# Performance work log

Hardware: AMD Instinct MI355X
Metric: run time of the kernel (lower is better)

## Reference

```python
import jax, jax.numpy as jnp
import numpy as np

N = 100000      # nodes
E = 1600000     # edges (avg degree 16)
D_IN, D_H, D_OUT = 128, 128, 64


def setup_inputs() -> dict:
    key = jax.random.key(0)
    k1, k2, k3, k4 = jax.random.split(key, 4)
    x = jax.random.normal(k1, (N, D_IN), dtype=jnp.float32)
    edge_index = jax.random.randint(k2, (2, E), 0, N, dtype=jnp.int32)
    W1 = jax.random.normal(k3, (D_IN, D_H), dtype=jnp.float32) * (1.0 / np.sqrt(D_IN))
    b1 = jnp.zeros((D_H,), dtype=jnp.float32)
    W2 = jax.random.normal(k4, (D_H, D_OUT), dtype=jnp.float32) * (1.0 / np.sqrt(D_H))
    b2 = jnp.zeros((D_OUT,), dtype=jnp.float32)
    return {"x": x, "edge_index": edge_index, "W1": W1, "b1": b1, "W2": W2, "b2": b2}


def _gcn_conv(x, src, dst, W, b):
    """PyG GCNConv: out = D^{-1/2} (A + I) D^{-1/2} (x W) + b."""
    n = x.shape[0]
    h = x @ W  # [N, D_out] — transform first, then aggregate (PyG order)
    loops = jnp.arange(n, dtype=src.dtype)
    src_f = jnp.concatenate([src, loops])
    dst_f = jnp.concatenate([dst, loops])
    deg = jax.ops.segment_sum(jnp.ones_like(dst_f, dtype=h.dtype), dst_f, num_segments=n)
    dinv = jax.lax.rsqrt(deg)  # deg >= 1 due to self-loops
    norm = dinv[src_f] * dinv[dst_f]            # [E+N]
    msg = h[src_f] * norm[:, None]              # [E+N, D_out] gather
    out = jax.ops.segment_sum(msg, dst_f, num_segments=n)  # scatter-add
    return out + b


def reference(x, edge_index, W1, b1, W2, b2):
    src, dst = edge_index[0], edge_index[1]
    h = jax.nn.relu(_gcn_conv(x, src, dst, W1, b1))
    o = _gcn_conv(h, src, dst, W2, b2)
    return jax.nn.log_softmax(o, axis=1)
```

## Files before the change

kernel.cpp:

```cpp
#include <hip/hip_runtime.h>
#include <hip/hip_bf16.h>

typedef __hip_bfloat16 bf16;
typedef short short8 __attribute__((ext_vector_type(8)));
typedef float f32x4 __attribute__((ext_vector_type(4)));
typedef float f32x2 __attribute__((ext_vector_type(2)));

#define NPB 256
#define MAXBUK 1024

__device__ __forceinline__ float bf2f_raw(unsigned short u) {
    unsigned x = ((unsigned)u) << 16; float f; __builtin_memcpy(&f, &x, 4); return f;
}
__device__ __forceinline__ unsigned short f2bf_raw(float f) {
    unsigned u; __builtin_memcpy(&u, &f, 4);
    u += 0x7FFFu + ((u >> 16) & 1u);
    return (unsigned short)(u >> 16);
}
__device__ __forceinline__ float lo_f(unsigned u) {
    unsigned x = u << 16; float f; __builtin_memcpy(&f, &x, 4); return f;
}
__device__ __forceinline__ float hi_f(unsigned u) {
    unsigned x = u & 0xffff0000u; float f; __builtin_memcpy(&f, &x, 4); return f;
}


__global__ __launch_bounds__(256) void fatA_kernel(const unsigned short* __restrict__ W1s,
                                                   const void* __restrict__ W1p,
                                                   const void* __restrict__ W2p,
                                                   const void* __restrict__ b1p,
                                                   const void* __restrict__ b2p,
                                                   unsigned short* __restrict__ WB1,
                                                   unsigned short* __restrict__ WB2,
                                                   float* __restrict__ b1f,
                                                   float* __restrict__ b2f,
                                                   int* __restrict__ flag, int nshorts,
                                                   const int* __restrict__ dst,
                                                   int* __restrict__ bktcnt,
                                                   int E, int nbuk, int prepb) {
    __shared__ int smem[MAXBUK];
    const int tt = threadIdx.x;
    if ((int)blockIdx.x < prepb) {
        const int sample = min(nshorts, 2048);
        int c = 0;
        for (int i = tt; i < sample; i += 256) {
            unsigned e = (W1s[i] >> 7) & 0xFFu;
            if (e >= 140u || (e >= 1u && e <= 40u)) c++;
        }
        smem[tt] = c;
        __syncthreads();
        for (int o = 128; o > 0; o >>= 1) {
            if (tt < o) smem[tt] += smem[tt + o];
            __syncthreads();
        }
        const int isf32 = (smem[0] > sample / 8) ? 1 : 0;
        if (blockIdx.x == 0 && tt == 0) *flag = isf32;

        const int t = blockIdx.x * 256 + tt;
        const int T1 = 16384, T2 = 8192;
        if (t < T1) {
            int j = t & 7, l = (t >> 3) & 63, f = t >> 9;
            int n = f >> 2, kk = f & 3;
            int k = kk * 32 + (l >> 4) * 8 + j;
            int col = n * 16 + (l & 15);
            WB1[t] = isf32 ? f2bf_raw(((const float*)W1p)[k * 128 + col])
                           : ((const unsigned short*)W1p)[k * 128 + col];
        } else if (t < T1 + T2) {
            int o = t - T1;
            int j = o & 7, l = (o >> 3) & 63, f = o >> 9;
            int n = f >> 2, kk = f & 3;
            int k = kk * 32 + (l >> 4) * 8 + j;
            int col = n * 16 + (l & 15);
            WB2[o] = isf32 ? f2bf_raw(((const float*)W2p)[k * 64 + col])
                           : ((const unsigned short*)W2p)[k * 64 + col];
        } else if (t < T1 + T2 + 128) {
            int o = t - T1 - T2;
            b1f[o] = isf32 ? ((const float*)b1p)[o] : bf2f_raw(((const unsigned short*)b1p)[o]);
        } else if (t < T1 + T2 + 192) {
            int o = t - T1 - T2 - 128;
            b2f[o] = isf32 ? ((const float*)b2p)[o] : bf2f_raw(((const unsigned short*)b2p)[o]);
        }
    } else {
        const int e0 = ((int)blockIdx.x - prepb) * 4096;
        const int e1 = min(E, e0 + 4096);
        for (int b = tt; b < nbuk; b += 256) smem[b] = 0;
        __syncthreads();
        for (int e = e0 + tt; e < e1; e += 256) atomicAdd(&smem[dst[e] >> 8], 1);
        __syncthreads();
        for (int b = tt; b < nbuk; b += 256) {
            int c = smem[b];
            if (c) atomicAdd(&bktcnt[b], c);
        }
    }
}

__global__ __launch_bounds__(1024) void bscan_kernel(const int* __restrict__ bktcnt,
                                                     int* __restrict__ bofs,
                                                     int* __restrict__ bcur,
                                                     int nbuk, int total) {
    __shared__ int ps[1024];
    const int t = threadIdx.x;
    int v = (t < nbuk) ? bktcnt[t] : 0;
    ps[t] = v;
    __syncthreads();
    for (int o = 1; o < 1024; o <<= 1) {
        int u = (t >= o) ? ps[t - o] : 0;
        __syncthreads();
        ps[t] += u;
        __syncthreads();
    }
    if (t < nbuk) {
        int ex = ps[t] - v;
        bofs[t] = ex;
        bcur[t] = ex;
    }
    if (t == 0) bofs[nbuk] = total;
}


__global__ __launch_bounds__(256) void fatB_kernel(const void* __restrict__ Xp,
                                                   const unsigned short* __restrict__ WB1,
                                                   unsigned char* __restrict__ Hf8, int nrows,
                                                   const int* __restrict__ flag,
                                                   const int* __restrict__ src,
                                                   const int* __restrict__ dst,
                                                   int* __restrict__ bcur,
                                                   unsigned* __restrict__ packed,
                                                   int E, int nbuk, int gb) {
    __shared__ __align__(16) char smem[34816];
    const int t = threadIdx.x;
    if ((int)blockIdx.x < gb) {
        unsigned short* Xs = (unsigned short*)smem;
        unsigned short* Cs = (unsigned short*)smem;
        const int r0 = blockIdx.x * 128;
        const int isf32 = *flag;

        if (isf32) {
            const float4* Xg = (const float4*)Xp;
            #pragma unroll
            for (int i = 0; i < 16; ++i) {
                int idx = t + 256 * i;
                int row = idx >> 5, c4 = idx & 31;
                float4 v = {0.f, 0.f, 0.f, 0.f};
                if (r0 + row < nrows) v = Xg[(size_t)(r0 + row) * 32 + c4];
                unsigned lo = (unsigned)f2bf_raw(v.x) | ((unsigned)f2bf_raw(v.y) << 16);
                unsigned hi = (unsigned)f2bf_raw(v.z) | ((unsigned)f2bf_raw(v.w) << 16);
                *reinterpret_cast<uint2*>(&Xs[row * 136 + c4 * 4]) = make_uint2(lo, hi);
            }
        } else {
            const uint4* Xg = (const uint4*)Xp;
            #pragma unroll
            for (int i = 0; i < 8; ++i) {
                int idx = t + 256 * i;
                int row = idx >> 4, c8 = idx & 15;
                uint4 v = {0u, 0u, 0u, 0u};
                if (r0 + row < nrows) v = Xg[(size_t)(r0 + row) * 16 + c8];
                *reinterpret_cast<uint4*>(&Xs[row * 136 + c8 * 8]) = v;
            }
        }
        __syncthreads();

        const int lane = t & 63, w = t >> 6;
        const int m0 = w * 32;
        short8 a[2][4];
        #pragma unroll
        for (int rt = 0; rt < 2; ++rt)
            #pragma unroll
            for (int kk = 0; kk < 4; ++kk)
                a[rt][kk] = *reinterpret_cast<const short8*>(
                    &Xs[(m0 + rt * 16 + (lane & 15)) * 136 + kk * 32 + (lane >> 4) * 8]);
        __syncthreads();

        for (int p = 0; p < 2; ++p) {
            short8 b[4][4];
            #pragma unroll
            for (int n = 0; n < 4; ++n)
                #pragma unroll
                for (int kk = 0; kk < 4; ++kk)
                    b[n][kk] = *reinterpret_cast<const short8*>(
                        WB1 + (size_t)(((p * 4 + n) * 4 + kk) * 64 + lane) * 8);
            f32x4 acc[2][4];
            #pragma unroll
            for (int rt = 0; rt < 2; ++rt)
                #pragma unroll
                for (int n = 0; n < 4; ++n) {
                    acc[rt][n] = (f32x4){0.f, 0.f, 0.f, 0.f};
                    #pragma unroll
                    for (int kk = 0; kk < 4; ++kk)
                        acc[rt][n] = __builtin_amdgcn_mfma_f32_16x16x32_bf16(
                            a[rt][kk], b[n][kk], acc[rt][n], 0, 0, 0);
                }
            if (p) __syncthreads();
            #pragma unroll
            for (int rt = 0; rt < 2; ++rt)
                #pragma unroll
                for (int n = 0; n < 4; ++n)
                    #pragma unroll
                    for (int r = 0; r < 4; ++r) {
                        int row = m0 + rt * 16 + (lane >> 4) * 4 + r;
                        Cs[row * 68 + n * 16 + (lane & 15)] = f2bf_raw(acc[rt][n][r]);
                    }
            __syncthreads();
            #pragma unroll
            for (int i = 0; i < 4; ++i) {
                int idx = t + 256 * i;
                int row = idx >> 3, c8 = idx & 7;
                if (r0 + row < nrows) {
                    uint2 va = *reinterpret_cast<const uint2*>(&Cs[row * 68 + c8 * 8]);
                    uint2 vb = *reinterpret_cast<const uint2*>(&Cs[row * 68 + c8 * 8 + 4]);
                    int w0 = __builtin_amdgcn_cvt_pk_fp8_f32(lo_f(va.x), hi_f(va.x), 0, false);
                    w0 = __builtin_amdgcn_cvt_pk_fp8_f32(lo_f(va.y), hi_f(va.y), w0, true);
                    int w1 = __builtin_amdgcn_cvt_pk_fp8_f32(lo_f(vb.x), hi_f(vb.x), 0, false);
                    w1 = __builtin_amdgcn_cvt_pk_fp8_f32(lo_f(vb.y), hi_f(vb.y), w1, true);
                    *reinterpret_cast<uint2*>(Hf8 + (size_t)(r0 + row) * 128 + p * 64 + c8 * 8) =
                        make_uint2((unsigned)w0, (unsigned)w1);
                }
            }
            if (!p) __syncthreads();
        }
    } else {
        int* cnt = (int*)smem;
        int* gbase = (int*)(smem + 4096);
        const int e0 = ((int)blockIdx.x - gb) * 4096;
        const int e1 = min(E, e0 + 4096);
        for (int b = t; b < nbuk; b += 256) cnt[b] = 0;
        __syncthreads();
        for (int e = e0 + t; e < e1; e += 256) atomicAdd(&cnt[dst[e] >> 8], 1);
        __syncthreads();
        for (int b = t; b < nbuk; b += 256) {
            int c = cnt[b];
            gbase[b] = c ? atomicAdd(&bcur[b], c) : 0;
            cnt[b] = 0;
        }
        __syncthreads();
        for (int e = e0 + t; e < e1; e += 256) {
            int d = dst[e];
            int b = d >> 8;
            int r = atomicAdd(&cnt[b], 1);
            packed[gbase[b] + r] = ((unsigned)(d & 255) << 24) | (unsigned)src[e];
        }
    }
}

__global__ __launch_bounds__(256) void csr_fine2_kernel(const unsigned* __restrict__ packed,
                                                        const int* __restrict__ bofs,
                                                        uint2* __restrict__ nmeta,
                                                        float* __restrict__ dinv,
                                                        unsigned* __restrict__ epu, int n) {
    __shared__ int cnt2[NPB];
    __shared__ int cur[NPB];
    const int t = threadIdx.x;
    const int b = blockIdx.x;
    const int node0 = b << 8;
    const int nn = min(NPB, n - node0);
    cnt2[t] = 0;
    __syncthreads();
    const int beg = bofs[b], end = bofs[b + 1];
    for (int i = beg + t; i < end; i += 256) atomicAdd(&cnt2[packed[i] >> 24], 1);
    __syncthreads();
    int c = cnt2[t];
    cur[t] = c;
    __syncthreads();
    for (int o = 1; o < 256; o <<= 1) {
        int u = (t >= o) ? cur[t - o] : 0;
        __syncthreads();
        cur[t] += u;
        __syncthreads();
    }
    const int base = beg + cur[t] - c;
    if (t < nn) {
        nmeta[node0 + t] = make_uint2((unsigned)base, (unsigned)c);
        dinv[node0 + t] = rsqrtf((float)(c + 1));
    }
    __syncthreads();
    cur[t] = base;
    __syncthreads();
    for (int i = beg + t; i < end; i += 256) {
        unsigned u = packed[i];
        int pos = atomicAdd(&cur[u >> 24], 1);
        epu[2 * pos] = u & 0xFFFFFFu;
    }
}

__global__ __launch_bounds__(256) void epw_kernel(unsigned* __restrict__ epu,
                                                  const float* __restrict__ dinv, int E) {
    int i = blockIdx.x * 256 + threadIdx.x;
    if (i < E) {
        unsigned s = epu[2 * i];
        float w = dinv[s];
        unsigned wb; __builtin_memcpy(&wb, &w, 4);
        epu[2 * i + 1] = wb;
    }
}


__device__ __forceinline__ float epw_f(uint2 e) {
    float w; __builtin_memcpy(&w, &e.y, 4); return w;
}

__device__ __forceinline__ void accf8_2(f32x2* acc, uint2 v, float w) {
    f32x2 wv = {w, w};
    acc[0] += __builtin_amdgcn_cvt_pk_f32_fp8(v.x, false) * wv;
    acc[1] += __builtin_amdgcn_cvt_pk_f32_fp8(v.x, true)  * wv;
    acc[2] += __builtin_amdgcn_cvt_pk_f32_fp8(v.y, false) * wv;
    acc[3] += __builtin_amdgcn_cvt_pk_f32_fp8(v.y, true)  * wv;
}

__global__ __launch_bounds__(128) void agg128_v9(const uint2* __restrict__ H2,
                                                 const uint2* __restrict__ nmeta,
                                                 const uint2* __restrict__ epack,
                                                 const float* __restrict__ biasf,
                                                 uint4* __restrict__ G4, int n) {
    const int lane = threadIdx.x & 63;
    const int g = lane >> 4;
    const int sub = lane & 15;
    const int node = blockIdx.x * 2 + (threadIdx.x >> 6);
    if (node >= n) return;

    uint2 vself = H2[((unsigned)node << 4) + (unsigned)sub];

    const uint2 meta = nmeta[node];
    const int base = (int)meta.x;
    const int cnt = (int)meta.y;
    const int end = base + cnt;
    const float di = rsqrtf((float)(cnt + 1));

    f32x2 acc[4];
    #pragma unroll
    for (int i = 0; i < 4; ++i) acc[i] = (f32x2){0.f, 0.f};
    accf8_2(acc, vself, (g == 0) ? di : 0.f);

    int j = base;
    for (; j + 15 < end; j += 16) {
        uint2 e0 = epack[j + g];
        uint2 e1 = epack[j + 4 + g];
        uint2 e2 = epack[j + 8 + g];
        uint2 e3 = epack[j + 12 + g];
        uint2 v0 = H2[(e0.x << 4) + (unsigned)sub];
        uint2 v1 = H2[(e1.x << 4) + (unsigned)sub];
        uint2 v2 = H2[(e2.x << 4) + (unsigned)sub];
        uint2 v3 = H2[(e3.x << 4) + (unsigned)sub];
        accf8_2(acc, v0, epw_f(e0));
        accf8_2(acc, v1, epw_f(e1));
        accf8_2(acc, v2, epw_f(e2));
        accf8_2(acc, v3, epw_f(e3));
    }
    for (; j + 7 < end; j += 8) {
        uint2 e0 = epack[j + g];
        uint2 e1 = epack[j + 4 + g];
        uint2 v0 = H2[(e0.x << 4) + (unsigned)sub];
        uint2 v1 = H2[(e1.x << 4) + (unsigned)sub];
        accf8_2(acc, v0, epw_f(e0));
        accf8_2(acc, v1, epw_f(e1));
    }
    for (; j + 3 < end; j += 4) {
        uint2 e0 = epack[j + g];
        uint2 v0 = H2[(e0.x << 4) + (unsigned)sub];
        accf8_2(acc, v0, epw_f(e0));
    }
    if (j + g < end) {
        uint2 e0 = epack[j + g];
        uint2 v0 = H2[(e0.x << 4) + (unsigned)sub];
        accf8_2(acc, v0, epw_f(e0));
    }

    float a8[8];
    #pragma unroll
    for (int i = 0; i < 4; ++i) { a8[2 * i] = acc[i].x; a8[2 * i + 1] = acc[i].y; }
    #pragma unroll
    for (int i = 0; i < 8; ++i) {
        a8[i] += __shfl_xor(a8[i], 16, 64);
        a8[i] += __shfl_xor(a8[i], 32, 64);
    }

    if (g == 0) {
        const float4* b4 = (const float4*)biasf;
        float4 blo = b4[sub * 2], bhi = b4[sub * 2 + 1];
        a8[0] = fmaxf(fmaf(di, a8[0], blo.x), 0.f);
        a8[1] = fmaxf(fmaf(di, a8[1], blo.y), 0.f);
        a8[2] = fmaxf(fmaf(di, a8[2], blo.z), 0.f);
        a8[3] = fmaxf(fmaf(di, a8[3], blo.w), 0.f);
        a8[4] = fmaxf(fmaf(di, a8[4], bhi.x), 0.f);
        a8[5] = fmaxf(fmaf(di, a8[5], bhi.y), 0.f);
        a8[6] = fmaxf(fmaf(di, a8[6], bhi.z), 0.f);
        a8[7] = fmaxf(fmaf(di, a8[7], bhi.w), 0.f);
        uint4 o;
        o.x = (unsigned)f2bf_raw(a8[0]) | ((unsigned)f2bf_raw(a8[1]) << 16);
        o.y = (unsigned)f2bf_raw(a8[2]) | ((unsigned)f2bf_raw(a8[3]) << 16);
        o.z = (unsigned)f2bf_raw(a8[4]) | ((unsigned)f2bf_raw(a8[5]) << 16);
        o.w = (unsigned)f2bf_raw(a8[6]) | ((unsigned)f2bf_raw(a8[7]) << 16);
        G4[((unsigned)node << 4) + (unsigned)sub] = o;
    }
}


__global__ __launch_bounds__(256) void gemm2b_mfma(const unsigned short* __restrict__ X,
                                                   const unsigned short* __restrict__ WB2,
                                                   unsigned short* __restrict__ T, int nrows) {
    __shared__ __align__(16) char smem[34816];
    unsigned short* Xs = (unsigned short*)smem;
    unsigned short* Cs = (unsigned short*)smem;
    const int t = threadIdx.x;
    const int r0 = blockIdx.x * 128;

    const uint4* Xg = (const uint4*)X;
    #pragma unroll
    for (int i = 0; i < 8; ++i) {
        int idx = t + 256 * i;
        int row = idx >> 4, c8 = idx & 15;
        uint4 v = {0u, 0u, 0u, 0u};
        if (r0 + row < nrows) v = Xg[(size_t)(r0 + row) * 16 + c8];
        *reinterpret_cast<uint4*>(&Xs[row * 136 + c8 * 8]) = v;
    }
    __syncthreads();

    const int lane = t & 63, w = t >> 6;
    const int m0 = w * 32;
    short8 a[2][4];
    #pragma unroll
    for (int rt = 0; rt < 2; ++rt)
        #pragma unroll
        for (int kk = 0; kk < 4; ++kk)
            a[rt][kk] = *reinterpret_cast<const short8*>(
                &Xs[(m0 + rt * 16 + (lane & 15)) * 136 + kk * 32 + (lane >> 4) * 8]);
    __syncthreads();

    short8 b[4][4];
    #pragma unroll
    for (int n = 0; n < 4; ++n)
        #pragma unroll
        for (int kk = 0; kk < 4; ++kk)
            b[n][kk] = *reinterpret_cast<const short8*>(
                WB2 + (size_t)((n * 4 + kk) * 64 + lane) * 8);

    f32x4 acc[2][4];
    #pragma unroll
    for (int rt = 0; rt < 2; ++rt)
        #pragma unroll
        for (int n = 0; n < 4; ++n) {
            acc[rt][n] = (f32x4){0.f, 0.f, 0.f, 0.f};
            #pragma unroll
            for (int kk = 0; kk < 4; ++kk)
                acc[rt][n] = __builtin_amdgcn_mfma_f32_16x16x32_bf16(
                    a[rt][kk], b[n][kk], acc[rt][n], 0, 0, 0);
        }

    #pragma unroll
    for (int rt = 0; rt < 2; ++rt)
        #pragma unroll
        for (int n = 0; n < 4; ++n)
            #pragma unroll
            for (int r = 0; r < 4; ++r) {
                int row = m0 + rt * 16 + (lane >> 4) * 4 + r;
                Cs[row * 68 + n * 16 + (lane & 15)] = f2bf_raw(acc[rt][n][r]);
            }
    __syncthreads();
    #pragma unroll
    for (int i = 0; i < 8; ++i) {
        int idx = t + 256 * i;
        int row = idx >> 4, c4 = idx & 15;
        if (r0 + row < nrows) {
            uint2 v = *reinterpret_cast<const uint2*>(&Cs[row * 68 + c4 * 4]);
            *reinterpret_cast<uint2*>(T + (size_t)(r0 + row) * 64 + c4 * 4) = v;
        }
    }
}


__device__ __forceinline__ void acc4v(f32x2* acc, uint2 v, float w) {
    f32x2 wv = {w, w};
    acc[0] += (f32x2){lo_f(v.x), hi_f(v.x)} * wv;
    acc[1] += (f32x2){lo_f(v.y), hi_f(v.y)} * wv;
}

__global__ __launch_bounds__(128) void agg64_final(const uint2* __restrict__ T2,
                                                   const uint2* __restrict__ nmeta,
                                                   const uint2* __restrict__ epack,
                                                   const float* __restrict__ b2f,
                                                   void* __restrict__ OUTv, int n,
                                                   const int* __restrict__ flag) {
    const int lane = threadIdx.x & 63;
    const int g = lane >> 4;
    const int sub = lane & 15;
    const int node = blockIdx.x * 2 + (threadIdx.x >> 6);
    if (node >= n) return;
    const int outf32 = *flag;

    uint2 vself = T2[((unsigned)node << 4) + (unsigned)sub];

    const uint2 meta = nmeta[node];
    const int base = (int)meta.x;
    const int cnt = (int)meta.y;
    const int end = base + cnt;
    const float di = rsqrtf((float)(cnt + 1));

    f32x2 acc[2];
    {
        const float ws = (g == 0) ? di : 0.f;
        acc[0] = (f32x2){ws * lo_f(vself.x), ws * hi_f(vself.x)};
        acc[1] = (f32x2){ws * lo_f(vself.y), ws * hi_f(vself.y)};
    }

    int j = base;
    for (; j + 15 < end; j += 16) {
        uint2 e0 = epack[j + g];
        uint2 e1 = epack[j + 4 + g];
        uint2 e2 = epack[j + 8 + g];
        uint2 e3 = epack[j + 12 + g];
        uint2 v0 = T2[(e0.x << 4) + (unsigned)sub];
        uint2 v1 = T2[(e1.x << 4) + (unsigned)sub];
        uint2 v2 = T2[(e2.x << 4) + (unsigned)sub];
        uint2 v3 = T2[(e3.x << 4) + (unsigned)sub];
        acc4v(acc, v0, epw_f(e0));
        acc4v(acc, v1, epw_f(e1));
        acc4v(acc, v2, epw_f(e2));
        acc4v(acc, v3, epw_f(e3));
    }
    for (; j + 7 < end; j += 8) {
        uint2 e0 = epack[j + g];
        uint2 e1 = epack[j + 4 + g];
        uint2 v0 = T2[(e0.x << 4) + (unsigned)sub];
        uint2 v1 = T2[(e1.x << 4) + (unsigned)sub];
        acc4v(acc, v0, epw_f(e0));
        acc4v(acc, v1, epw_f(e1));
    }
    for (; j + 3 < end; j += 4) {
        uint2 e0 = epack[j + g];
        uint2 v0 = T2[(e0.x << 4) + (unsigned)sub];
        acc4v(acc, v0, epw_f(e0));
    }
    if (j + g < end) {
        uint2 e0 = epack[j + g];
        uint2 v0 = T2[(e0.x << 4) + (unsigned)sub];
        acc4v(acc, v0, epw_f(e0));
    }

    float a4[4] = {acc[0].x, acc[0].y, acc[1].x, acc[1].y};
    #pragma unroll
    for (int i = 0; i < 4; ++i) {
        a4[i] += __shfl_xor(a4[i], 16, 64);
        a4[i] += __shfl_xor(a4[i], 32, 64);
    }

    if (g == 0) {
        float4 bb = ((const float4*)b2f)[sub];
        a4[0] = fmaf(di, a4[0], bb.x);
        a4[1] = fmaf(di, a4[1], bb.y);
        a4[2] = fmaf(di, a4[2], bb.z);
        a4[3] = fmaf(di, a4[3], bb.w);

        float m = fmaxf(fmaxf(a4[0], a4[1]), fmaxf(a4[2], a4[3]));
        m = fmaxf(m, __shfl_xor(m, 1, 64));
        m = fmaxf(m, __shfl_xor(m, 2, 64));
        m = fmaxf(m, __shfl_xor(m, 4, 64));
        m = fmaxf(m, __shfl_xor(m, 8, 64));
        float s = __expf(a4[0] - m) + __expf(a4[1] - m) +
                  __expf(a4[2] - m) + __expf(a4[3] - m);
        s += __shfl_xor(s, 1, 64);
        s += __shfl_xor(s, 2, 64);
        s += __shfl_xor(s, 4, 64);
        s += __shfl_xor(s, 8, 64);
        const float lse = m + __logf(s);

        if (outf32) {
            float4 o = {a4[0] - lse, a4[1] - lse, a4[2] - lse, a4[3] - lse};
            ((float4*)OUTv)[(size_t)node * 16 + sub] = o;
        } else {
            uint2 o;
            o.x = (unsigned)f2bf_raw(a4[0] - lse) | ((unsigned)f2bf_raw(a4[1] - lse) << 16);
            o.y = (unsigned)f2bf_raw(a4[2] - lse) | ((unsigned)f2bf_raw(a4[3] - lse) << 16);
            ((uint2*)OUTv)[(size_t)node * 16 + sub] = o;
        }
    }
}


extern "C" void kernel_launch(void* const* d_in, const int* in_sizes, int n_in,
                              void* d_out, int out_size, void* d_ws, size_t ws_size,
                              hipStream_t stream) {
    const void* x  = d_in[0];
    const int*  ei = (const int*)d_in[1];
    const void* W1 = d_in[2];
    const void* b1 = d_in[3];
    const void* W2 = d_in[4];
    const void* b2 = d_in[5];

    const int N = in_sizes[0] / 128;
    const int E = in_sizes[1] / 2;
    const int* src = ei;
    const int* dst = ei + E;
    const int NBUK = (N + NPB - 1) / NPB;

    char* p = (char*)d_ws;
    auto alloc = [&](size_t bytes) { char* q = p; p += (bytes + 255) & ~255ull; return q; };
    int*   flag   = (int*)  alloc(4);
    uint2* nmeta  = (uint2*)alloc((size_t)N * 8);
    float* dinv   = (float*)alloc((size_t)N * 4);
    int*   bktcnt = (int*)  alloc((size_t)NBUK * 4);
    int*   bofs   = (int*)  alloc((size_t)(NBUK + 1) * 4);
    int*   bcur   = (int*)  alloc((size_t)NBUK * 4);
    float* b1f    = (float*)alloc(128 * 4);
    float* b2f    = (float*)alloc(64 * 4);
    unsigned short* WB1 = (unsigned short*)alloc(16384 * 2);
    unsigned short* WB2 = (unsigned short*)alloc(8192 * 2);
    unsigned* big = (unsigned*)alloc((size_t)N * 128 * 2);
    unsigned* packed = (unsigned*)d_out;
    uint2*    epack  = (uint2*)d_in[1];
    unsigned* g1 = (unsigned*)d_in[0];
    unsigned short* T = (unsigned short*)big;
    (void)ws_size; (void)n_in; (void)out_size;

    const int PREPB = 97;
    const int MSB = (E + 4095) / 4096;
    const int GB = (N + 127) / 128;

    hipMemsetAsync(bktcnt, 0, (size_t)NBUK * 4, stream);
    fatA_kernel<<<PREPB + MSB, 256, 0, stream>>>((const unsigned short*)W1, W1, W2, b1, b2,
                                                 WB1, WB2, b1f, b2f, flag, in_sizes[2],
                                                 dst, bktcnt, E, NBUK, PREPB);
    bscan_kernel<<<1, 1024, 0, stream>>>(bktcnt, bofs, bcur, NBUK, E);
    fatB_kernel<<<GB + MSB, 256, 0, stream>>>(x, WB1, (unsigned char*)big, N, flag,
                                              src, dst, bcur, packed, E, NBUK, GB);
    csr_fine2_kernel<<<NBUK, 256, 0, stream>>>(packed, bofs, nmeta, dinv, (unsigned*)epack, N);
    epw_kernel<<<(E + 255) / 256, 256, 0, stream>>>((unsigned*)epack, dinv, E);

    agg128_v9<<<(N + 1) / 2, 128, 0, stream>>>((const uint2*)big, nmeta, epack, b1f, (uint4*)g1, N);
    gemm2b_mfma<<<GB, 256, 0, stream>>>((const unsigned short*)g1, WB2, T, N);
    agg64_final<<<(N + 1) / 2, 128, 0, stream>>>((const uint2*)T, nmeta, epack, b2f, d_out, N, flag);
}
```

Before: 294.0 us.

## Fold source-side normalization into GEMM epilogues and drop per-edge weights

Scales each GEMM output row by dinv[row] before storing, so the aggregation kernels sum plain neighbor rows and only apply the destination dinv at the end. This removes the epw_kernel pass and shrinks the edge list from 8-byte (src, weight) pairs to 4-byte source indices, halving index traffic in both aggregations. In exchange, GEMM1 can no longer overlap with the CSR bucket scatter inside one fused kernel, because it now waits for dinv from csr_fine2. Scaling before the fp8 quantization also shifts the rounding error slightly.

```diff
diff --git a/kernel.cpp b/kernel.cpp
--- a/kernel.cpp
+++ b/kernel.cpp
@@ -117,128 +117,31 @@
     if (t == 0) bofs[nbuk] = total;
 }
 
-
-__global__ __launch_bounds__(256) void fatB_kernel(const void* __restrict__ Xp,
-                                                   const unsigned short* __restrict__ WB1,
-                                                   unsigned char* __restrict__ Hf8, int nrows,
-                                                   const int* __restrict__ flag,
-                                                   const int* __restrict__ src,
-                                                   const int* __restrict__ dst,
-                                                   int* __restrict__ bcur,
-                                                   unsigned* __restrict__ packed,
-                                                   int E, int nbuk, int gb) {
-    __shared__ __align__(16) char smem[34816];
+__global__ __launch_bounds__(256) void ms_scatter_kernel(const int* __restrict__ src,
+                                                         const int* __restrict__ dst,
+                                                         int* __restrict__ bcur,
+                                                         unsigned* __restrict__ packed,
+                                                         int E, int nbuk) {
+    __shared__ int cnt[MAXBUK];
+    __shared__ int gbase[MAXBUK];
     const int t = threadIdx.x;
-    if ((int)blockIdx.x < gb) {
-        unsigned short* Xs = (unsigned short*)smem;
-        unsigned short* Cs = (unsigned short*)smem;
-        const int r0 = blockIdx.x * 128;
-        const int isf32 = *flag;
-
-        if (isf32) {
-            const float4* Xg = (const float4*)Xp;
-            #pragma unroll
-            for (int i = 0; i < 16; ++i) {
-                int idx = t + 256 * i;
-                int row = idx >> 5, c4 = idx & 31;
-                float4 v = {0.f, 0.f, 0.f, 0.f};
-                if (r0 + row < nrows) v = Xg[(size_t)(r0 + row) * 32 + c4];
-                unsigned lo = (unsigned)f2bf_raw(v.x) | ((unsigned)f2bf_raw(v.y) << 16);
-                unsigned hi = (unsigned)f2bf_raw(v.z) | ((unsigned)f2bf_raw(v.w) << 16);
-                *reinterpret_cast<uint2*>(&Xs[row * 136 + c4 * 4]) = make_uint2(lo, hi);
-            }
-        } else {
-            const uint4* Xg = (const uint4*)Xp;
-            #pragma unroll
-            for (int i = 0; i < 8; ++i) {
-                int idx = t + 256 * i;
-                int row = idx >> 4, c8 = idx & 15;
-                uint4 v = {0u, 0u, 0u, 0u};
-                if (r0 + row < nrows) v = Xg[(size_t)(r0 + row) * 16 + c8];
-                *reinterpret_cast<uint4*>(&Xs[row * 136 + c8 * 8]) = v;
-            }
-        }
-        __syncthreads();
-
-        const int lane = t & 63, w = t >> 6;
-        const int m0 = w * 32;
-        short8 a[2][4];
-        #pragma unroll
-        for (int rt = 0; rt < 2; ++rt)
-            #pragma unroll
-            for (int kk = 0; kk < 4; ++kk)
-                a[rt][kk] = *reinterpret_cast<const short8*>(
-                    &Xs[(m0 + rt * 16 + (lane & 15)) * 136 + kk * 32 + (lane >> 4) * 8]);
-        __syncthreads();
-
-        for (int p = 0; p < 2; ++p) {
-            short8 b[4][4];
-            #pragma unroll
-            for (int n = 0; n < 4; ++n)
-                #pragma unroll
-                for (int kk = 0; kk < 4; ++kk)
-                    b[n][kk] = *reinterpret_cast<const short8*>(
-                        WB1 + (size_t)(((p * 4 + n) * 4 + kk) * 64 + lane) * 8);
-            f32x4 acc[2][4];
-            #pragma unroll
-            for (int rt = 0; rt < 2; ++rt)
-                #pragma unroll
-                for (int n = 0; n < 4; ++n) {
-                    acc[rt][n] = (f32x4){0.f, 0.f, 0.f, 0.f};
-                    #pragma unroll
-                    for (int kk = 0; kk < 4; ++kk)
-                        acc[rt][n] = __builtin_amdgcn_mfma_f32_16x16x32_bf16(
-                            a[rt][kk], b[n][kk], acc[rt][n], 0, 0, 0);
-                }
-            if (p) __syncthreads();
-            #pragma unroll
-            for (int rt = 0; rt < 2; ++rt)
-                #pragma unroll
-                for (int n = 0; n < 4; ++n)
-                    #pragma unroll
-                    for (int r = 0; r < 4; ++r) {
-                        int row = m0 + rt * 16 + (lane >> 4) * 4 + r;
-                        Cs[row * 68 + n * 16 + (lane & 15)] = f2bf_raw(acc[rt][n][r]);
-                    }
-            __syncthreads();
-            #pragma unroll
-            for (int i = 0; i < 4; ++i) {
-                int idx = t + 256 * i;
-                int row = idx >> 3, c8 = idx & 7;
-                if (r0 + row < nrows) {
-                    uint2 va = *reinterpret_cast<const uint2*>(&Cs[row * 68 + c8 * 8]);
-                    uint2 vb = *reinterpret_cast<const uint2*>(&Cs[row * 68 + c8 * 8 + 4]);
-                    int w0 = __builtin_amdgcn_cvt_pk_fp8_f32(lo_f(va.x), hi_f(va.x), 0, false);
-                    w0 = __builtin_amdgcn_cvt_pk_fp8_f32(lo_f(va.y), hi_f(va.y), w0, true);
-                    int w1 = __builtin_amdgcn_cvt_pk_fp8_f32(lo_f(vb.x), hi_f(vb.x), 0, false);
-                    w1 = __builtin_amdgcn_cvt_pk_fp8_f32(lo_f(vb.y), hi_f(vb.y), w1, true);
-                    *reinterpret_cast<uint2*>(Hf8 + (size_t)(r0 + row) * 128 + p * 64 + c8 * 8) =
-                        make_uint2((unsigned)w0, (unsigned)w1);
-                }
-            }
-            if (!p) __syncthreads();
-        }
-    } else {
-        int* cnt = (int*)smem;
-        int* gbase = (int*)(smem + 4096);
-        const int e0 = ((int)blockIdx.x - gb) * 4096;
-        const int e1 = min(E, e0 + 4096);
-        for (int b = t; b < nbuk; b += 256) cnt[b] = 0;
-        __syncthreads();
-        for (int e = e0 + t; e < e1; e += 256) atomicAdd(&cnt[dst[e] >> 8], 1);
-        __syncthreads();
-        for (int b = t; b < nbuk; b += 256) {
-            int c = cnt[b];
-            gbase[b] = c ? atomicAdd(&bcur[b], c) : 0;
-            cnt[b] = 0;
-        }
-        __syncthreads();
-        for (int e = e0 + t; e < e1; e += 256) {
-            int d = dst[e];
-            int b = d >> 8;
-            int r = atomicAdd(&cnt[b], 1);
-            packed[gbase[b] + r] = ((unsigned)(d & 255) << 24) | (unsigned)src[e];
-        }
+    const int e0 = blockIdx.x * 4096;
+    const int e1 = min(E, e0 + 4096);
+    for (int b = t; b < nbuk; b += 256) cnt[b] = 0;
+    __syncthreads();
+    for (int e = e0 + t; e < e1; e += 256) atomicAdd(&cnt[dst[e] >> 8], 1);
+    __syncthreads();
+    for (int b = t; b < nbuk; b += 256) {
+        int c = cnt[b];
+        gbase[b] = c ? atomicAdd(&bcur[b], c) : 0;
+        cnt[b] = 0;
+    }
+    __syncthreads();
+    for (int e = e0 + t; e < e1; e += 256) {
+        int d = dst[e];
+        int b = d >> 8;
+        int r = atomicAdd(&cnt[b], 1);
+        packed[gbase[b] + r] = ((unsigned)(d & 255) << 24) | (unsigned)src[e];
     }
 }
 
@@ -246,7 +149,7 @@
                                                         const int* __restrict__ bofs,
                                                         uint2* __restrict__ nmeta,
                                                         float* __restrict__ dinv,
-                                                        unsigned* __restrict__ epu, int n) {
+                                                        int* __restrict__ csrc, int n) {
     __shared__ int cnt2[NPB];
     __shared__ int cur[NPB];
     const int t = threadIdx.x;
@@ -278,39 +181,122 @@
     for (int i = beg + t; i < end; i += 256) {
         unsigned u = packed[i];
         int pos = atomicAdd(&cur[u >> 24], 1);
-        epu[2 * pos] = u & 0xFFFFFFu;
-    }
-}
-
-__global__ __launch_bounds__(256) void epw_kernel(unsigned* __restrict__ epu,
-                                                  const float* __restrict__ dinv, int E) {
-    int i = blockIdx.x * 256 + threadIdx.x;
-    if (i < E) {
-        unsigned s = epu[2 * i];
-        float w = dinv[s];
-        unsigned wb; __builtin_memcpy(&wb, &w, 4);
-        epu[2 * i + 1] = wb;
-    }
-}
-
-
-__device__ __forceinline__ float epw_f(uint2 e) {
-    float w; __builtin_memcpy(&w, &e.y, 4); return w;
-}
-
-__device__ __forceinline__ void accf8_2(f32x2* acc, uint2 v, float w) {
-    f32x2 wv = {w, w};
-    acc[0] += __builtin_amdgcn_cvt_pk_f32_fp8(v.x, false) * wv;
-    acc[1] += __builtin_amdgcn_cvt_pk_f32_fp8(v.x, true)  * wv;
-    acc[2] += __builtin_amdgcn_cvt_pk_f32_fp8(v.y, false) * wv;
-    acc[3] += __builtin_amdgcn_cvt_pk_f32_fp8(v.y, true)  * wv;
-}
-
-__global__ __launch_bounds__(128) void agg128_v9(const uint2* __restrict__ H2,
-                                                 const uint2* __restrict__ nmeta,
-                                                 const uint2* __restrict__ epack,
-                                                 const float* __restrict__ biasf,
-                                                 uint4* __restrict__ G4, int n) {
+        csrc[pos] = (int)(u & 0xFFFFFFu);
+    }
+}
+
+
+__global__ __launch_bounds__(256) void gemm1p_mfma(const void* __restrict__ Xp,
+                                                   const unsigned short* __restrict__ WB1,
+                                                   const float* __restrict__ dinv,
+                                                   unsigned char* __restrict__ Hf8, int nrows,
+                                                   const int* __restrict__ flag) {
+    __shared__ __align__(16) char smem[34816];
+    unsigned short* Xs = (unsigned short*)smem;
+    unsigned short* Cs = (unsigned short*)smem;
+    const int t = threadIdx.x;
+    const int r0 = blockIdx.x * 128;
+    const int isf32 = *flag;
+
+    if (isf32) {
+        const float4* Xg = (const float4*)Xp;
+        #pragma unroll
+        for (int i = 0; i < 16; ++i) {
+            int idx = t + 256 * i;
+            int row = idx >> 5, c4 = idx & 31;
+            float4 v = {0.f, 0.f, 0.f, 0.f};
+            if (r0 + row < nrows) v = Xg[(size_t)(r0 + row) * 32 + c4];
+            unsigned lo = (unsigned)f2bf_raw(v.x) | ((unsigned)f2bf_raw(v.y) << 16);
+            unsigned hi = (unsigned)f2bf_raw(v.z) | ((unsigned)f2bf_raw(v.w) << 16);
+            *reinterpret_cast<uint2*>(&Xs[row * 136 + c4 * 4]) = make_uint2(lo, hi);
+        }
+    } else {
+        const uint4* Xg = (const uint4*)Xp;
+        #pragma unroll
+        for (int i = 0; i < 8; ++i) {
+            int idx = t + 256 * i;
+            int row = idx >> 4, c8 = idx & 15;
+            uint4 v = {0u, 0u, 0u, 0u};
+            if (r0 + row < nrows) v = Xg[(size_t)(r0 + row) * 16 + c8];
+            *reinterpret_cast<uint4*>(&Xs[row * 136 + c8 * 8]) = v;
+        }
+    }
+    __syncthreads();
+
+    const int lane = t & 63, w = t >> 6;
+    const int m0 = w * 32;
+    short8 a[2][4];
+    #pragma unroll
+    for (int rt = 0; rt < 2; ++rt)
+        #pragma unroll
+        for (int kk = 0; kk < 4; ++kk)
+            a[rt][kk] = *reinterpret_cast<const short8*>(
+                &Xs[(m0 + rt * 16 + (lane & 15)) * 136 + kk * 32 + (lane >> 4) * 8]);
+    __syncthreads();
+
+    for (int p = 0; p < 2; ++p) {
+        short8 b[4][4];
+        #pragma unroll
+        for (int n = 0; n < 4; ++n)
+            #pragma unroll
+            for (int kk = 0; kk < 4; ++kk)
+                b[n][kk] = *reinterpret_cast<const short8*>(
+                    WB1 + (size_t)(((p * 4 + n) * 4 + kk) * 64 + lane) * 8);
+        f32x4 acc[2][4];
+        #pragma unroll
+        for (int rt = 0; rt < 2; ++rt)
+            #pragma unroll
+            for (int n = 0; n < 4; ++n) {
+                acc[rt][n] = (f32x4){0.f, 0.f, 0.f, 0.f};
+                #pragma unroll
+                for (int kk = 0; kk < 4; ++kk)
+                    acc[rt][n] = __builtin_amdgcn_mfma_f32_16x16x32_bf16(
+                        a[rt][kk], b[n][kk], acc[rt][n], 0, 0, 0);
+            }
+        if (p) __syncthreads();
+        #pragma unroll
+        for (int rt = 0; rt < 2; ++rt)
+            #pragma unroll
+            for (int n = 0; n < 4; ++n)
+                #pragma unroll
+                for (int r = 0; r < 4; ++r) {
+                    int row = m0 + rt * 16 + (lane >> 4) * 4 + r;
+                    Cs[row * 68 + n * 16 + (lane & 15)] = f2bf_raw(acc[rt][n][r]);
+                }
+        __syncthreads();
+        #pragma unroll
+        for (int i = 0; i < 4; ++i) {
+            int idx = t + 256 * i;
+            int row = idx >> 3, c8 = idx & 7;
+            if (r0 + row < nrows) {
+                float dv = dinv[r0 + row];
+                uint2 va = *reinterpret_cast<const uint2*>(&Cs[row * 68 + c8 * 8]);
+                uint2 vb = *reinterpret_cast<const uint2*>(&Cs[row * 68 + c8 * 8 + 4]);
+                int w0 = __builtin_amdgcn_cvt_pk_fp8_f32(dv * lo_f(va.x), dv * hi_f(va.x), 0, false);
+                w0 = __builtin_amdgcn_cvt_pk_fp8_f32(dv * lo_f(va.y), dv * hi_f(va.y), w0, true);
+                int w1 = __builtin_amdgcn_cvt_pk_fp8_f32(dv * lo_f(vb.x), dv * hi_f(vb.x), 0, false);
+                w1 = __builtin_amdgcn_cvt_pk_fp8_f32(dv * lo_f(vb.y), dv * hi_f(vb.y), w1, true);
+                *reinterpret_cast<uint2*>(Hf8 + (size_t)(r0 + row) * 128 + p * 64 + c8 * 8) =
+                    make_uint2((unsigned)w0, (unsigned)w1);
+            }
+        }
+        if (!p) __syncthreads();
+    }
+}
+
+
+__device__ __forceinline__ void accf8_nw(f32x2* acc, uint2 v) {
+    acc[0] += __builtin_amdgcn_cvt_pk_f32_fp8(v.x, false);
+    acc[1] += __builtin_amdgcn_cvt_pk_f32_fp8(v.x, true);
+    acc[2] += __builtin_amdgcn_cvt_pk_f32_fp8(v.y, false);
+    acc[3] += __builtin_amdgcn_cvt_pk_f32_fp8(v.y, true);
+}
+
+__global__ __launch_bounds__(128) void agg128_v10(const uint2* __restrict__ H2,
+                                                  const uint2* __restrict__ nmeta,
+                                                  const int* __restrict__ csrc,
+                                                  const float* __restrict__ biasf,
+                                                  uint4* __restrict__ G4, int n) {
     const int lane = threadIdx.x & 63;
     const int g = lane >> 4;
     const int sub = lane & 15;
@@ -328,40 +314,40 @@
     f32x2 acc[4];
     #pragma unroll
     for (int i = 0; i < 4; ++i) acc[i] = (f32x2){0.f, 0.f};
-    accf8_2(acc, vself, (g == 0) ? di : 0.f);
+    if (g == 0) accf8_nw(acc, vself);
 
     int j = base;
     for (; j + 15 < end; j += 16) {
-        uint2 e0 = epack[j + g];
-        uint2 e1 = epack[j + 4 + g];
-        uint2 e2 = epack[j + 8 + g];
-        uint2 e3 = epack[j + 12 + g];
-        uint2 v0 = H2[(e0.x << 4) + (unsigned)sub];
-        uint2 v1 = H2[(e1.x << 4) + (unsigned)sub];
-        uint2 v2 = H2[(e2.x << 4) + (unsigned)sub];
-        uint2 v3 = H2[(e3.x << 4) + (unsigned)sub];
-        accf8_2(acc, v0, epw_f(e0));
-        accf8_2(acc, v1, epw_f(e1));
-        accf8_2(acc, v2, epw_f(e2));
-        accf8_2(acc, v3, epw_f(e3));
+        int s0 = csrc[j + g];
+        int s1 = csrc[j + 4 + g];
+        int s2 = csrc[j + 8 + g];
+        int s3 = csrc[j + 12 + g];
+        uint2 v0 = H2[((unsigned)s0 << 4) + (unsigned)sub];
+        uint2 v1 = H2[((unsigned)s1 << 4) + (unsigned)sub];
+        uint2 v2 = H2[((unsigned)s2 << 4) + (unsigned)sub];
+        uint2 v3 = H2[((unsigned)s3 << 4) + (unsigned)sub];
+        accf8_nw(acc, v0);
+        accf8_nw(acc, v1);
+        accf8_nw(acc, v2);
+        accf8_nw(acc, v3);
     }
     for (; j + 7 < end; j += 8) {
-        uint2 e0 = epack[j + g];
-        uint2 e1 = epack[j + 4 + g];
-        uint2 v0 = H2[(e0.x << 4) + (unsigned)sub];
-        uint2 v1 = H2[(e1.x << 4) + (unsigned)sub];
-        accf8_2(acc, v0, epw_f(e0));
-        accf8_2(acc, v1, epw_f(e1));
+        int s0 = csrc[j + g];
+        int s1 = csrc[j + 4 + g];
+        uint2 v0 = H2[((unsigned)s0 << 4) + (unsigned)sub];
+        uint2 v1 = H2[((unsigned)s1 << 4) + (unsigned)sub];
+        accf8_nw(acc, v0);
+        accf8_nw(acc, v1);
     }
     for (; j + 3 < end; j += 4) {
-        uint2 e0 = epack[j + g];
-        uint2 v0 = H2[(e0.x << 4) + (unsigned)sub];
-        accf8_2(acc, v0, epw_f(e0));
+        int s0 = csrc[j + g];
+        uint2 v0 = H2[((unsigned)s0 << 4) + (unsigned)sub];
+        accf8_nw(acc, v0);
     }
     if (j + g < end) {
-        uint2 e0 = epack[j + g];
-        uint2 v0 = H2[(e0.x << 4) + (unsigned)sub];
-        accf8_2(acc, v0, epw_f(e0));
+        int s0 = csrc[j + g];
+        uint2 v0 = H2[((unsigned)s0 << 4) + (unsigned)sub];
+        accf8_nw(acc, v0);
     }
 
     float a8[8];
@@ -394,9 +380,10 @@
 }
 
 
-__global__ __launch_bounds__(256) void gemm2b_mfma(const unsigned short* __restrict__ X,
-                                                   const unsigned short* __restrict__ WB2,
-                                                   unsigned short* __restrict__ T, int nrows) {
+__global__ __launch_bounds__(256) void gemm2bp_mfma(const unsigned short* __restrict__ X,
+                                                    const unsigned short* __restrict__ WB2,
+                                                    const float* __restrict__ dinv,
+                                                    unsigned short* __restrict__ T, int nrows) {
     __shared__ __align__(16) char smem[34816];
     unsigned short* Xs = (unsigned short*)smem;
     unsigned short* Cs = (unsigned short*)smem;
@@ -460,25 +447,29 @@
         int idx = t + 256 * i;
         int row = idx >> 4, c4 = idx & 15;
         if (r0 + row < nrows) {
+            float dv = dinv[r0 + row];
             uint2 v = *reinterpret_cast<const uint2*>(&Cs[row * 68 + c4 * 4]);
-            *reinterpret_cast<uint2*>(T + (size_t)(r0 + row) * 64 + c4 * 4) = v;
-        }
-    }
-}
-
-
-__device__ __forceinline__ void acc4v(f32x2* acc, uint2 v, float w) {
-    f32x2 wv = {w, w};
-    acc[0] += (f32x2){lo_f(v.x), hi_f(v.x)} * wv;
-    acc[1] += (f32x2){lo_f(v.y), hi_f(v.y)} * wv;
-}
-
-__global__ __launch_bounds__(128) void agg64_final(const uint2* __restrict__ T2,
-                                                   const uint2* __restrict__ nmeta,
-                                                   const uint2* __restrict__ epack,
-                                                   const float* __restrict__ b2f,
-                                                   void* __restrict__ OUTv, int n,
-                                                   const int* __restrict__ flag) {
+            unsigned ox = (unsigned)f2bf_raw(dv * lo_f(v.x)) |
+                          ((unsigned)f2bf_raw(dv * hi_f(v.x)) << 16);
+            unsigned oy = (unsigned)f2bf_raw(dv * lo_f(v.y)) |
+                          ((unsigned)f2bf_raw(dv * hi_f(v.y)) << 16);
+            *reinterpret_cast<uint2*>(T + (size_t)(r0 + row) * 64 + c4 * 4) = make_uint2(ox, oy);
+        }
+    }
+}
+
+
+__device__ __forceinline__ void acc4v_nw(f32x2* acc, uint2 v) {
+    acc[0] += (f32x2){lo_f(v.x), hi_f(v.x)};
+    acc[1] += (f32x2){lo_f(v.y), hi_f(v.y)};
+}
+
+__global__ __launch_bounds__(128) void agg64_v3(const uint2* __restrict__ T2,
+                                                const uint2* __restrict__ nmeta,
+                                                const int* __restrict__ csrc,
+                                                const float* __restrict__ b2f,
+                                                void* __restrict__ OUTv, int n,
+                                                const int* __restrict__ flag) {
     const int lane = threadIdx.x & 63;
     const int g = lane >> 4;
     const int sub = lane & 15;
@@ -495,44 +486,42 @@
     const float di = rsqrtf((float)(cnt + 1));
 
     f32x2 acc[2];
-    {
-        const float ws = (g == 0) ? di : 0.f;
-        acc[0] = (f32x2){ws * lo_f(vself.x), ws * hi_f(vself.x)};
-        acc[1] = (f32x2){ws * lo_f(vself.y), ws * hi_f(vself.y)};
-    }
+    acc[0] = (f32x2){0.f, 0.f};
+    acc[1] = (f32x2){0.f, 0.f};
+    if (g == 0) acc4v_nw(acc, vself);
 
     int j = base;
     for (; j + 15 < end; j += 16) {
-        uint2 e0 = epack[j + g];
-        uint2 e1 = epack[j + 4 + g];
-        uint2 e2 = epack[j + 8 + g];
-        uint2 e3 = epack[j + 12 + g];
-        uint2 v0 = T2[(e0.x << 4) + (unsigned)sub];
-        uint2 v1 = T2[(e1.x << 4) + (unsigned)sub];
-        uint2 v2 = T2[(e2.x << 4) + (unsigned)sub];
-        uint2 v3 = T2[(e3.x << 4) + (unsigned)sub];
-        acc4v(acc, v0, epw_f(e0));
-        acc4v(acc, v1, epw_f(e1));
-        acc4v(acc, v2, epw_f(e2));
-        acc4v(acc, v3, epw_f(e3));
+        int s0 = csrc[j + g];
+        int s1 = csrc[j + 4 + g];
+        int s2 = csrc[j + 8 + g];
+        int s3 = csrc[j + 12 + g];
+        uint2 v0 = T2[((unsigned)s0 << 4) + (unsigned)sub];
+        uint2 v1 = T2[((unsigned)s1 << 4) + (unsigned)sub];
+        uint2 v2 = T2[((unsigned)s2 << 4) + (unsigned)sub];
+        uint2 v3 = T2[((unsigned)s3 << 4) + (unsigned)sub];
+        acc4v_nw(acc, v0);
+        acc4v_nw(acc, v1);
+        acc4v_nw(acc, v2);
+        acc4v_nw(acc, v3);
     }
     for (; j + 7 < end; j += 8) {
-        uint2 e0 = epack[j + g];
-        uint2 e1 = epack[j + 4 + g];
-        uint2 v0 = T2[(e0.x << 4) + (unsigned)sub];
-        uint2 v1 = T2[(e1.x << 4) + (unsigned)sub];
-        acc4v(acc, v0, epw_f(e0));
-        acc4v(acc, v1, epw_f(e1));
+        int s0 = csrc[j + g];
+        int s1 = csrc[j + 4 + g];
+        uint2 v0 = T2[((unsigned)s0 << 4) + (unsigned)sub];
+        uint2 v1 = T2[((unsigned)s1 << 4) + (unsigned)sub];
+        acc4v_nw(acc, v0);
+        acc4v_nw(acc, v1);
     }
     for (; j + 3 < end; j += 4) {
-        uint2 e0 = epack[j + g];
-        uint2 v0 = T2[(e0.x << 4) + (unsigned)sub];
-        acc4v(acc, v0, epw_f(e0));
+        int s0 = csrc[j + g];
+        uint2 v0 = T2[((unsigned)s0 << 4) + (unsigned)sub];
+        acc4v_nw(acc, v0);
     }
     if (j + g < end) {
-        uint2 e0 = epack[j + g];
-        uint2 v0 = T2[(e0.x << 4) + (unsigned)sub];
-        acc4v(acc, v0, epw_f(e0));
+        int s0 = csrc[j + g];
+        uint2 v0 = T2[((unsigned)s0 << 4) + (unsigned)sub];
+        acc4v_nw(acc, v0);
     }
 
     float a4[4] = {acc[0].x, acc[0].y, acc[1].x, acc[1].y};
@@ -605,7 +594,7 @@
     unsigned short* WB2 = (unsigned short*)alloc(8192 * 2);
     unsigned* big = (unsigned*)alloc((size_t)N * 128 * 2);
     unsigned* packed = (unsigned*)d_out;
-    uint2*    epack  = (uint2*)d_in[1];
+    int*      csrc   = (int*)d_in[1];
     unsigned* g1 = (unsigned*)d_in[0];
     unsigned short* T = (unsigned short*)big;
     (void)ws_size; (void)n_in; (void)out_size;
@@ -619,12 +608,11 @@
                                                  WB1, WB2, b1f, b2f, flag, in_sizes[2],
                                                  dst, bktcnt, E, NBUK, PREPB);
     bscan_kernel<<<1, 1024, 0, stream>>>(bktcnt, bofs, bcur, NBUK, E);
-    fatB_kernel<<<GB + MSB, 256, 0, stream>>>(x, WB1, (unsigned char*)big, N, flag,
-                                              src, dst, bcur, packed, E, NBUK, GB);
-    csr_fine2_kernel<<<NBUK, 256, 0, stream>>>(packed, bofs, nmeta, dinv, (unsigned*)epack, N);
-    epw_kernel<<<(E + 255) / 256, 256, 0, stream>>>((unsigned*)epack, dinv, E);
-
-    agg128_v9<<<(N + 1) / 2, 128, 0, stream>>>((const uint2*)big, nmeta, epack, b1f, (uint4*)g1, N);
-    gemm2b_mfma<<<GB, 256, 0, stream>>>((const unsigned short*)g1, WB2, T, N);
-    agg64_final<<<(N + 1) / 2, 128, 0, stream>>>((const uint2*)T, nmeta, epack, b2f, d_out, N, flag);
-}
+    ms_scatter_kernel<<<MSB, 256, 0, stream>>>(src, dst, bcur, packed, E, NBUK);
+    csr_fine2_kernel<<<NBUK, 256, 0, stream>>>(packed, bofs, nmeta, dinv, csrc, N);
+
+    gemm1p_mfma<<<GB, 256, 0, stream>>>(x, WB1, dinv, (unsigned char*)big, N, flag);
+    agg128_v10<<<(N + 1) / 2, 128, 0, stream>>>((const uint2*)big, nmeta, csrc, b1f, (uint4*)g1, N);
+    gemm2bp_mfma<<<GB, 256, 0, stream>>>((const unsigned short*)g1, WB2, dinv, T, N);
+    agg64_v3<<<(N + 1) / 2, 128, 0, stream>>>((const uint2*)T, nmeta, csrc, b2f, d_out, N, flag);
+}
```

New measurement: 280.7 us (median of 2 runs). 1.05x faster.
